# Performance work log

Hardware: AMD Instinct MI355X
Metric: run time of the kernel (lower is better)

Reference implementation:

```python
import jax, jax.numpy as jnp
import numpy as np

N = 65536        # collocation points
IN_DIM = 4       # x_dim=3 + is_unsteady=1
DEPTH = 256      # hidden width ('depth' arg)
HID = 5          # width-1 hidden tanh layers
OUT = 3


def setup_inputs() -> dict:
    key = jax.random.key(0)
    ks = jax.random.split(key, 4)
    def init(k, shape, fan_in):
        return jax.random.normal(k, shape, dtype=jnp.float32) / np.sqrt(fan_in).astype(np.float32)
    return {
        "x":  jax.random.normal(ks[0], (N, IN_DIM), dtype=jnp.float32),
        "W0": init(ks[1], (IN_DIM, DEPTH), IN_DIM),
        "b0": jnp.zeros((DEPTH,), jnp.float32),
        "Wh": init(ks[2], (HID, DEPTH, DEPTH), DEPTH),
        "bh": jnp.zeros((HID, DEPTH), jnp.float32),
        "Wl": init(ks[3], (DEPTH, OUT), DEPTH),
        "bl": jnp.zeros((OUT,), jnp.float32),
    }


def _mlp(x, W0, b0, Wh, bh, Wl, bl):
    # Faithful to nn.Sequential: first Linear has NO activation after it,
    # then (width-1) x [Linear, Tanh], then output Linear.
    h = x @ W0 + b0
    for i in range(HID):
        h = jnp.tanh(h @ Wh[i] + bh[i])
    return h @ Wl + bl  # vector potential a: [N, 3]


def reference(x, W0, b0, Wh, bh, Wl, bl):
    # curl(a) via 3 batched reverse-mode pulls (same math as torch autograd.grad
    # with grad_outputs = e_i repeated over the batch).
    a, vjp_fn = jax.vjp(lambda xx: _mlp(xx, W0, b0, Wh, bh, Wl, bl), x)
    e = jnp.eye(OUT, dtype=x.dtype)
    cots = jnp.broadcast_to(e[:, None, :], (OUT, x.shape[0], OUT))  # [3, N, 3]
    J = jax.vmap(lambda c: vjp_fn(c)[0])(cots)                      # [3, N, IN_DIM]
    da0dx, da1dx, da2dx = J[0], J[1], J[2]
    u = jnp.stack([
        da2dx[:, 1] - da1dx[:, 2],
        da0dx[:, 2] - da2dx[:, 0],
        da1dx[:, 0] - da0dx[:, 1],
    ], axis=1)  # [N, 3]
    return u
```

## Files before the change

kernel.cpp:

```cpp
#include <hip/hip_runtime.h>

typedef _Float16 f16;
typedef _Float16 f16x4 __attribute__((ext_vector_type(4)));
typedef _Float16 f16x8 __attribute__((ext_vector_type(8)));
typedef float    f32x4 __attribute__((ext_vector_type(4)));

#define OFF_WHP   0u
#define OFF_WLP   655360u
#define OFF_W0P   663552u
#define OFF_B0P   729088u
#define OFF_GP    745472u
#define OFF_BHP   794624u

__device__ __forceinline__ int phi(int kk, int g, int e){
  return (kk*2 + (e>>2))*16 + g*4 + (e&3);
}

__device__ __forceinline__ float tanh_fast(float z){
  float e = __builtin_amdgcn_exp2f(z * 2.885390081777927f);
  return 1.f - 2.f*__builtin_amdgcn_rcpf(e + 1.f);
}

__global__ void prepack(const float* __restrict__ W0, const float* __restrict__ b0,
                        const float* __restrict__ Wh, const float* __restrict__ bh,
                        const float* __restrict__ Wl, unsigned char* __restrict__ ws){
  int tid = blockIdx.x*256 + threadIdx.x;
  f16*   whp = (f16*)(ws + OFF_WHP);
  f16*   wlp = (f16*)(ws + OFF_WLP);
  float* w0p = (float*)(ws + OFF_W0P);
  float* b0p = (float*)(ws + OFF_B0P);
  float* gp  = (float*)(ws + OFF_GP);
  float* bhp = (float*)(ws + OFF_BHP);
  if (tid < 327680){
    int e=tid&7, lane=(tid>>3)&63, kk=(tid>>9)&7, nt=(tid>>12)&15, l=tid>>16;
    int k = phi(kk, lane>>4, e);
    int n = nt*16 + (lane&15);
    whp[tid] = (f16)Wh[(l*256 + k)*256 + n];
  } else if (tid < 331776){
    int t = tid - 327680;
    int e=t&7, lane=(t>>3)&63, kk=t>>9;
    int k = phi(kk, lane>>4, e);
    int n = lane&15;
    wlp[t] = (n<3) ? (f16)Wl[k*3+n] : (f16)0.f;
  } else if (tid < 335872){
    int t = tid - 331776;
    int e=t&7, lane=(t>>3)&63, kk=t>>9;
    int k = phi(kk, lane>>4, e);
    #pragma unroll
    for(int i=0;i<4;i++) w0p[t*4+i] = W0[i*256+k];
    b0p[t] = b0[k];
  } else if (tid < 348160){
    int t = tid - 335872;
    int e=t&7, lane=(t>>3)&63, kk=(t>>9)&7, j=t>>12;
    int k = phi(kk, lane>>4, e);
    float acc = 0.f;
    for(int k0=0;k0<256;k0++) acc = fmaf(W0[j*256+k0], Wh[k0*256+k], acc);
    gp[t] = acc;
  } else if (tid < 368640){
    int t = tid - 348160;
    int r=t&3, lane=(t>>2)&63, nt=(t>>8)&15, l=t>>12;
    bhp[t] = bh[l*256 + nt*16 + (lane>>4)*4 + r];
  }
}

__device__ __forceinline__ int moff(int s, int n){
  return ((s<<9) + (n<<1)) ^ ((s&7)<<4);
}

__global__ __launch_bounds__(256, 2) void velcurl(
    const float* __restrict__ x, const unsigned char* __restrict__ ws,
    float* __restrict__ out){
  __shared__ __align__(16) char mbuf[2][8192];
  __shared__ float outt[3][3][16];

  const int lane  = threadIdx.x & 63;
  const int w     = threadIdx.x >> 6;
  const int s     = lane & 15;
  const int g     = lane >> 4;
  const int sbase = blockIdx.x << 4;

  const f16x8* __restrict__ whp = (const f16x8*)(ws + OFF_WHP);
  const f16x8* __restrict__ wlp = (const f16x8*)(ws + OFF_WLP);
  const f32x4* __restrict__ w0p = (const f32x4*)(ws + OFF_W0P);
  const float* __restrict__ b0p = (const float*)(ws + OFF_B0P);
  const float* __restrict__ gp  = (const float*)(ws + OFF_GP);
  const f32x4* __restrict__ bhp = (const f32x4*)(ws + OFF_BHP);

  f16x8 st[8];
  f16x8 nst[8];

  if (w==0){
    const f32x4 xv = ((const f32x4*)x)[sbase + s];
    #pragma unroll
    for(int kk=0;kk<8;kk++){
      f16x8 v;
      #pragma unroll
      for(int e=0;e<8;e++){
        f32x4 wv = w0p[(kk*64+lane)*8+e];
        float b  = b0p[(kk*64+lane)*8+e];
        float h = fmaf(xv[3],wv[3], fmaf(xv[2],wv[2], fmaf(xv[1],wv[1], fmaf(xv[0],wv[0], b))));
        v[e] = (f16)h;
      }
      st[kk] = v;
    }
    #pragma unroll
    for(int nt=0;nt<16;nt++){
      f32x4 acc = {0.f,0.f,0.f,0.f};
      #pragma unroll
      for(int kk=0;kk<8;kk++)
        acc = __builtin_amdgcn_mfma_f32_16x16x32_f16(whp[(nt*8+kk)*64+lane], st[kk], acc, 0,0,0);
      f32x4 bv = bhp[nt*64+lane];
      f16x4 mv;
      #pragma unroll
      for(int r=0;r<4;r++){
        float h = tanh_fast(acc[r]+bv[r]);
        nst[nt>>1][(nt&1)*4+r] = (f16)h;
        mv[r] = (f16)(1.f - h*h);
      }
      *(f16x4*)(&mbuf[0][0] + moff(s, nt*16 + 4*g)) = mv;
    }
    #pragma unroll
    for(int kk=0;kk<8;kk++) st[kk]=nst[kk];
  }
  __syncthreads();

  #pragma unroll 1
  for(int p=1;p<5;p++){
    const f16x8* wl = whp + p*8192;
    if (w==0){
      const f32x4* bp = bhp + p*1024;
      char* mb = &mbuf[p&1][0];
      #pragma unroll
      for(int nt=0;nt<16;nt++){
        f32x4 acc = {0.f,0.f,0.f,0.f};
        #pragma unroll
        for(int kk=0;kk<8;kk++)
          acc = __builtin_amdgcn_mfma_f32_16x16x32_f16(wl[(nt*8+kk)*64+lane], st[kk], acc, 0,0,0);
        f32x4 bv = bp[nt*64+lane];
        f16x4 mv;
        #pragma unroll
        for(int r=0;r<4;r++){
          float h = tanh_fast(acc[r]+bv[r]);
          nst[nt>>1][(nt&1)*4+r] = (f16)h;
          mv[r] = (f16)(1.f - h*h);
        }
        *(f16x4*)(mb + moff(s, nt*16 + 4*g)) = mv;
      }
      #pragma unroll
      for(int kk=0;kk<8;kk++) st[kk]=nst[kk];
    } else {
      const char* mb = &mbuf[(p-1)&1][0];
      f16x8 bf[8];
      if (p==1){
        const int j = w-1;
        #pragma unroll
        for(int kk=0;kk<8;kk++){
          f16x4 mlo = *(const f16x4*)(mb + moff(s,(2*kk+0)*16+4*g));
          f16x4 mhi = *(const f16x4*)(mb + moff(s,(2*kk+1)*16+4*g));
          f16x4 lo, hi;
          #pragma unroll
          for(int r=0;r<4;r++){
            lo[r] = (f16)((float)mlo[r] * gp[((j*8+kk)*64+lane)*8 + r]);
            hi[r] = (f16)((float)mhi[r] * gp[((j*8+kk)*64+lane)*8 + 4 + r]);
          }
          bf[kk] = __builtin_shufflevector(lo, hi, 0,1,2,3,4,5,6,7);
        }
      } else {
        #pragma unroll
        for(int kk=0;kk<8;kk++){
          f16x4 mlo = *(const f16x4*)(mb + moff(s,(2*kk+0)*16+4*g));
          f16x4 mhi = *(const f16x4*)(mb + moff(s,(2*kk+1)*16+4*g));
          f16x8 m8 = __builtin_shufflevector(mlo, mhi, 0,1,2,3,4,5,6,7);
          bf[kk] = m8 * nst[kk];
        }
      }
      #pragma unroll
      for(int nt=0;nt<16;nt++){
        f32x4 acc = {0.f,0.f,0.f,0.f};
        #pragma unroll
        for(int kk=0;kk<8;kk++)
          acc = __builtin_amdgcn_mfma_f32_16x16x32_f16(wl[(nt*8+kk)*64+lane], bf[kk], acc, 0,0,0);
        #pragma unroll
        for(int r=0;r<4;r++) nst[nt>>1][(nt&1)*4+r] = (f16)acc[r];
      }
    }
    __syncthreads();
  }

  if (w>0){
    const char* mb = &mbuf[0][0];
    f16x8 bf[8];
    #pragma unroll
    for(int kk=0;kk<8;kk++){
      f16x4 mlo = *(const f16x4*)(mb + moff(s,(2*kk+0)*16+4*g));
      f16x4 mhi = *(const f16x4*)(mb + moff(s,(2*kk+1)*16+4*g));
      f16x8 m8 = __builtin_shufflevector(mlo, mhi, 0,1,2,3,4,5,6,7);
      bf[kk] = m8 * nst[kk];
    }
    f32x4 acc = {0.f,0.f,0.f,0.f};
    #pragma unroll
    for(int kk=0;kk<8;kk++)
      acc = __builtin_amdgcn_mfma_f32_16x16x32_f16(wlp[kk*64+lane], bf[kk], acc, 0,0,0);
    if (lane<16){
      outt[w-1][0][lane] = acc[0];
      outt[w-1][1][lane] = acc[1];
      outt[w-1][2][lane] = acc[2];
    }
  }
  __syncthreads();

  if (w==0 && lane<16){
    const int so = (sbase + lane)*3;
    out[so+0] = outt[1][2][lane] - outt[2][1][lane];
    out[so+1] = outt[2][0][lane] - outt[0][2][lane];
    out[so+2] = outt[0][1][lane] - outt[1][0][lane];
  }
}

extern "C" void kernel_launch(void* const* d_in, const int* in_sizes, int n_in,
                              void* d_out, int out_size, void* d_ws, size_t ws_size,
                              hipStream_t stream){
  const float* x  = (const float*)d_in[0];
  const float* W0 = (const float*)d_in[1];
  const float* b0 = (const float*)d_in[2];
  const float* Wh = (const float*)d_in[3];
  const float* bh = (const float*)d_in[4];
  const float* Wl = (const float*)d_in[5];
  prepack<<<1440, 256, 0, stream>>>(W0, b0, Wh, bh, Wl, (unsigned char*)d_ws);
  velcurl<<<4096, 256, 0, stream>>>(x, (const unsigned char*)d_ws, (float*)d_out);
}
```

Before: 387.0 us.

## Store tanh derivatives as per-lane 16-byte LDS chunks and raise occupancy

Changes the shared-memory layout of the tanh-derivative buffer so each lane writes and reads one 16-byte f16x8 chunk per k-block, XOR-swizzled by lane to avoid bank conflicts. This replaces the paired 8-byte stores and loads with single wide accesses. The layout matches the register fragment order, so no shuffles are needed. It also raises the launch bounds from 2 to 4 blocks per CU, which lowers the register budget per thread and risks spills given the large f16x8 arrays held in registers.

```diff
diff --git a/kernel.cpp b/kernel.cpp
--- a/kernel.cpp
+++ b/kernel.cpp
@@ -63,11 +63,11 @@
   }
 }
 
-__device__ __forceinline__ int moff(int s, int n){
-  return ((s<<9) + (n<<1)) ^ ((s&7)<<4);
-}
-
-__global__ __launch_bounds__(256, 2) void velcurl(
+__device__ __forceinline__ int moff(int lane, int kk){
+  return lane*128 + ((kk ^ (lane & 7)) << 4);
+}
+
+__global__ __launch_bounds__(256, 4) void velcurl(
     const float* __restrict__ x, const unsigned char* __restrict__ ws,
     float* __restrict__ out){
   __shared__ __align__(16) char mbuf[2][8192];
@@ -76,7 +76,6 @@
   const int lane  = threadIdx.x & 63;
   const int w     = threadIdx.x >> 6;
   const int s     = lane & 15;
-  const int g     = lane >> 4;
   const int sbase = blockIdx.x << 4;
 
   const f16x8* __restrict__ whp = (const f16x8*)(ws + OFF_WHP);
@@ -103,6 +102,7 @@
       }
       st[kk] = v;
     }
+    f16x8 mc;
     #pragma unroll
     for(int nt=0;nt<16;nt++){
       f32x4 acc = {0.f,0.f,0.f,0.f};
@@ -110,14 +110,13 @@
       for(int kk=0;kk<8;kk++)
         acc = __builtin_amdgcn_mfma_f32_16x16x32_f16(whp[(nt*8+kk)*64+lane], st[kk], acc, 0,0,0);
       f32x4 bv = bhp[nt*64+lane];
-      f16x4 mv;
       #pragma unroll
       for(int r=0;r<4;r++){
         float h = tanh_fast(acc[r]+bv[r]);
         nst[nt>>1][(nt&1)*4+r] = (f16)h;
-        mv[r] = (f16)(1.f - h*h);
-      }
-      *(f16x4*)(&mbuf[0][0] + moff(s, nt*16 + 4*g)) = mv;
+        mc[(nt&1)*4+r] = (f16)(1.f - h*h);
+      }
+      if (nt&1) *(f16x8*)(&mbuf[0][0] + moff(lane, nt>>1)) = mc;
     }
     #pragma unroll
     for(int kk=0;kk<8;kk++) st[kk]=nst[kk];
@@ -130,6 +129,7 @@
     if (w==0){
       const f32x4* bp = bhp + p*1024;
       char* mb = &mbuf[p&1][0];
+      f16x8 mc;
       #pragma unroll
       for(int nt=0;nt<16;nt++){
         f32x4 acc = {0.f,0.f,0.f,0.f};
@@ -137,14 +137,13 @@
         for(int kk=0;kk<8;kk++)
           acc = __builtin_amdgcn_mfma_f32_16x16x32_f16(wl[(nt*8+kk)*64+lane], st[kk], acc, 0,0,0);
         f32x4 bv = bp[nt*64+lane];
-        f16x4 mv;
         #pragma unroll
         for(int r=0;r<4;r++){
           float h = tanh_fast(acc[r]+bv[r]);
           nst[nt>>1][(nt&1)*4+r] = (f16)h;
-          mv[r] = (f16)(1.f - h*h);
+          mc[(nt&1)*4+r] = (f16)(1.f - h*h);
         }
-        *(f16x4*)(mb + moff(s, nt*16 + 4*g)) = mv;
+        if (nt&1) *(f16x8*)(mb + moff(lane, nt>>1)) = mc;
       }
       #pragma unroll
       for(int kk=0;kk<8;kk++) st[kk]=nst[kk];
@@ -155,22 +154,17 @@
         const int j = w-1;
         #pragma unroll
         for(int kk=0;kk<8;kk++){
-          f16x4 mlo = *(const f16x4*)(mb + moff(s,(2*kk+0)*16+4*g));
-          f16x4 mhi = *(const f16x4*)(mb + moff(s,(2*kk+1)*16+4*g));
-          f16x4 lo, hi;
+          f16x8 m8 = *(const f16x8*)(mb + moff(lane, kk));
+          f16x8 v;
           #pragma unroll
-          for(int r=0;r<4;r++){
-            lo[r] = (f16)((float)mlo[r] * gp[((j*8+kk)*64+lane)*8 + r]);
-            hi[r] = (f16)((float)mhi[r] * gp[((j*8+kk)*64+lane)*8 + 4 + r]);
-          }
-          bf[kk] = __builtin_shufflevector(lo, hi, 0,1,2,3,4,5,6,7);
+          for(int e=0;e<8;e++)
+            v[e] = (f16)((float)m8[e] * gp[((j*8+kk)*64+lane)*8 + e]);
+          bf[kk] = v;
         }
       } else {
         #pragma unroll
         for(int kk=0;kk<8;kk++){
-          f16x4 mlo = *(const f16x4*)(mb + moff(s,(2*kk+0)*16+4*g));
-          f16x4 mhi = *(const f16x4*)(mb + moff(s,(2*kk+1)*16+4*g));
-          f16x8 m8 = __builtin_shufflevector(mlo, mhi, 0,1,2,3,4,5,6,7);
+          f16x8 m8 = *(const f16x8*)(mb + moff(lane, kk));
           bf[kk] = m8 * nst[kk];
         }
       }
@@ -189,18 +183,13 @@
 
   if (w>0){
     const char* mb = &mbuf[0][0];
-    f16x8 bf[8];
+    f32x4 acc = {0.f,0.f,0.f,0.f};
     #pragma unroll
     for(int kk=0;kk<8;kk++){
-      f16x4 mlo = *(const f16x4*)(mb + moff(s,(2*kk+0)*16+4*g));
-      f16x4 mhi = *(const f16x4*)(mb + moff(s,(2*kk+1)*16+4*g));
-      f16x8 m8 = __builtin_shufflevector(mlo, mhi, 0,1,2,3,4,5,6,7);
-      bf[kk] = m8 * nst[kk];
-    }
-    f32x4 acc = {0.f,0.f,0.f,0.f};
-    #pragma unroll
-    for(int kk=0;kk<8;kk++)
-      acc = __builtin_amdgcn_mfma_f32_16x16x32_f16(wlp[kk*64+lane], bf[kk], acc, 0,0,0);
+      f16x8 m8 = *(const f16x8*)(mb + moff(lane, kk));
+      f16x8 bf = m8 * nst[kk];
+      acc = __builtin_amdgcn_mfma_f32_16x16x32_f16(wlp[kk*64+lane], bf, acc, 0,0,0);
+    }
     if (lane<16){
       outt[w-1][0][lane] = acc[0];
       outt[w-1][1][lane] = acc[1];
```

After: 745.1 us. 1.93x slower.
